# Performance work log

Measured on AMD Instinct MI355X. Metric: run time of the kernel, lower is better.

The kernel has to match this reference:

```python
import jax, jax.numpy as jnp
import numpy as np

M_TOKENS, D_IN, D_OUT = 4096, 4096, 16384


def setup_inputs() -> dict:
    key = jax.random.key(0)
    k1, k2, k3, k4 = jax.random.split(key, 4)
    x = jax.random.normal(k1, (M_TOKENS, D_IN), dtype=jnp.float32)
    # pre-quantized int8 weight, stored [K, N] as in qweight_kn
    qweight_kn = jax.random.randint(k2, (D_IN, D_OUT), -127, 128, dtype=jnp.int8)
    # per-output-channel weight dequant scales (float16 buffer, used as fp32 in kernel)
    weight_scales = jax.random.uniform(k3, (D_OUT,), dtype=jnp.float32, minval=1e-3, maxval=2e-2)
    bias = jax.random.normal(k4, (D_OUT,), dtype=jnp.float32) * 0.01
    return {"x": x, "qweight_kn": qweight_kn, "weight_scales": weight_scales, "bias": bias}


def reference(x, qweight_kn, weight_scales, bias):
    target_dtype = x.dtype
    x2 = x.reshape(-1, x.shape[-1])  # [M, K]
    # dynamic per-token (per-row) symmetric quantization
    x_max = jnp.max(jnp.abs(x2), axis=-1, keepdims=True).astype(jnp.float32) + 1e-5
    x_scales = x_max / 127.0  # [M, 1]
    x_int8 = jnp.clip(jnp.round(x2.astype(jnp.float32) / x_scales), -128, 127).astype(jnp.int8)
    acc = jax.lax.dot_general(
        x_int8, qweight_kn,
        dimension_numbers=(((1,), (0,)), ((), ())),
        preferred_element_type=jnp.int32,
    )  # [M, N] int32
    # fused dequant: row act-scale * col weight-scale, plus bias
    c = acc.astype(jnp.float32) * x_scales * weight_scales[None, :].astype(jnp.float32)
    c = c + bias[None, :]
    out = c.astype(jnp.bfloat16)  # kernel stores bf16
    return out.reshape(*x.shape[:-1], -1).astype(target_dtype)
```

## Files before the change

### kernel.cpp

```cpp
#include <hip/hip_runtime.h>
#include <hip/hip_bf16.h>
#include <stdint.h>

typedef int v4i __attribute__((ext_vector_type(4)));

#define GM 4096
#define GN 16384
#define GK 4096
#define BM 256
#define BN 256
#define BK 64
#define NT (GK / BK)

__device__ __forceinline__ void gload16(const void* g, void* l) {
  __builtin_amdgcn_global_load_lds(
      (const __attribute__((address_space(1))) void*)g,
      (__attribute__((address_space(3))) void*)l, 16, 0, 0);
}

__global__ __launch_bounds__(256) void quant_rows(
    const float* __restrict__ x, int8_t* __restrict__ xq,
    float* __restrict__ xs, int K) {
  const int row = blockIdx.x;
  const int t = threadIdx.x;
  const float4* src = (const float4*)(x + (size_t)row * K) + t * 4;
  float4 v[4];
  float m = 0.f;
#pragma unroll
  for (int i = 0; i < 4; ++i) {
    v[i] = src[i];
    m = fmaxf(m, fmaxf(fmaxf(fabsf(v[i].x), fabsf(v[i].y)),
                       fmaxf(fabsf(v[i].z), fabsf(v[i].w))));
  }
#pragma unroll
  for (int off = 1; off < 64; off <<= 1)
    m = fmaxf(m, __shfl_xor(m, off, 64));
  __shared__ float wmax[4];
  if ((t & 63) == 0) wmax[t >> 6] = m;
  __syncthreads();
  const float gm = fmaxf(fmaxf(wmax[0], wmax[1]), fmaxf(wmax[2], wmax[3]));
  const float scale = (gm + 1e-5f) / 127.0f;
  if (t == 0) xs[row] = scale;
  unsigned packed[4];
#pragma unroll
  for (int i = 0; i < 4; ++i) {
    float fv[4] = {v[i].x, v[i].y, v[i].z, v[i].w};
    unsigned p = 0;
#pragma unroll
    for (int j = 0; j < 4; ++j) {
      int q = (int)rintf(fv[j] / scale);
      q = max(-128, min(127, q));
      p |= (unsigned)(q & 0xff) << (8 * j);
    }
    packed[i] = p;
  }
  *(int4*)(xq + (size_t)row * K + t * 16) =
      make_int4((int)packed[0], (int)packed[1], (int)packed[2], (int)packed[3]);
}

__global__ __launch_bounds__(256) void transpose_pack(
    const int* __restrict__ W32, int8_t* __restrict__ Wt2, int K, int N) {
  __shared__ __align__(16) int8_t tile[64][80];
  const int t = threadIdx.x;
  const int n0 = blockIdx.x * 64;
  const int k0 = blockIdx.y * 64;
  const int ln = t & 63;
  const int wv = t >> 6;
#pragma unroll
  for (int it = 0; it < 16; ++it) {
    const int kk = wv * 16 + it;
    tile[ln][kk] = (int8_t)W32[(size_t)(k0 + kk) * N + n0 + ln];
  }
  __syncthreads();
  const int lane = ln;
  const int4 v = *(const int4*)&tile[wv * 16 + (lane & 15)][(lane >> 4) * 16];
  const int tn = n0 >> 8;
  const int kt = k0 >> 6;
  const int f = ((n0 >> 4) & 15) + wv;
  *(int4*)(Wt2 + (((size_t)(tn * 64 + kt) * 16 + f) * 64 + lane) * 16) = v;
}

__global__ __launch_bounds__(512, 2) void gemm_i8(
    const int8_t* __restrict__ Xq, const int8_t* __restrict__ Wt2,
    const float* __restrict__ xs, const float* __restrict__ wsc,
    const float* __restrict__ bias, float* __restrict__ C) {
  __shared__ __align__(16) int8_t lA[4][BM * BK];

  const int t = threadIdx.x;
  const int lane = t & 63;
  const int w = t >> 6;
  const int wr = w >> 2;
  const int wc = w & 3;
  const int fr = lane & 15;
  const int kg = lane >> 4;

  const int bid = blockIdx.x;
  const int xcd = bid & 7;
  const int q = bid >> 3;
  const int tm = q & 15;
  const int tn = xcd * 8 + (q >> 4);
  const size_t rowA0 = (size_t)tm * BM;
  const size_t rowB0 = (size_t)tn * BN;

  const int8_t* XqB = Xq + rowA0 * GK;
  int srcOff[2], dstOff[2];
#pragma unroll
  for (int i = 0; i < 2; ++i) {
    const int slot0 = (w * 2 + i) * 64;
    const int slot = slot0 + lane;
    const int r = slot >> 2;
    const int c = (slot & 3) ^ ((r >> 2) & 3);
    srcOff[i] = r * GK + c * 16;
    dstOff[i] = slot0 * 16;
  }

#define STAGE(KT, SLOT)                                              \
  {                                                                  \
    const int ko = (KT)*BK;                                          \
    _Pragma("unroll") for (int i = 0; i < 2; ++i)                    \
        gload16(XqB + srcOff[i] + ko, &lA[(SLOT)][0] + dstOff[i]);   \
  }

  const int8_t* bq = Wt2 + (size_t)tn * 1048576 + wc * 4096 + lane * 16;

  v4i acc[8][4] = {};
  v4i areg[8], breg[4][4];

#define LOADB(KT, S)                                                          \
  {                                                                           \
    const int8_t* bp = bq + (size_t)(KT)*16384;                               \
    _Pragma("unroll") for (int nj = 0; nj < 4; ++nj)                          \
        asm volatile("global_load_dwordx4 %0, %1, off"                        \
                     : "=v"(breg[S][nj])                                      \
                     : "v"(bp + nj * 1024)                                    \
                     : "memory");                                             \
  }

  const int ckk = (kg ^ (fr >> 2)) * 16;
#define RD_A(MI, SLOT)                                                        \
  areg[MI] = *(const v4i*)&lA[(SLOT)][(wr * 128 + (MI)*16 + fr) * BK + ckk];

#define SB __builtin_amdgcn_sched_barrier(0)

#define BODY(T, SLOT)                                                         \
  {                                                                           \
         \
    asm volatile("s_waitcnt vmcnt(12)" ::: "memory");                         \
    __builtin_amdgcn_s_barrier();       \
    SB;                                                                       \
    STAGE(((T) + 3) & (NT - 1), ((SLOT) + 3) & 3);                            \
    LOADB(((T) + 3) & (NT - 1), ((SLOT) + 3) & 3);                            \
    SB;                                                                       \
    RD_A(0, SLOT); RD_A(1, SLOT); RD_A(2, SLOT); RD_A(3, SLOT);               \
    SB;                                                                       \
    RD_A(4, SLOT); RD_A(5, SLOT); RD_A(6, SLOT); RD_A(7, SLOT);               \
    SB;                                                                       \
    asm volatile("s_waitcnt lgkmcnt(4)" ::: "memory");        \
    SB;                                                                       \
    __builtin_amdgcn_s_setprio(1);                                            \
    _Pragma("unroll") for (int mi = 0; mi < 4; ++mi)                          \
        _Pragma("unroll") for (int nj = 0; nj < 4; ++nj)                      \
            acc[mi][nj] = __builtin_amdgcn_mfma_i32_16x16x64_i8(              \
                areg[mi], breg[SLOT][nj], acc[mi][nj], 0, 0, 0);              \
    __builtin_amdgcn_s_setprio(0);                                            \
    asm volatile("s_waitcnt lgkmcnt(0)" ::: "memory");        \
    SB;                                                                       \
    __builtin_amdgcn_s_setprio(1);                                            \
    _Pragma("unroll") for (int mi = 4; mi < 8; ++mi)                          \
        _Pragma("unroll") for (int nj = 0; nj < 4; ++nj)                      \
            acc[mi][nj] = __builtin_amdgcn_mfma_i32_16x16x64_i8(              \
                areg[mi], breg[SLOT][nj], acc[mi][nj], 0, 0, 0);              \
    __builtin_amdgcn_s_setprio(0);                                            \
  }

  STAGE(0, 0);
  LOADB(0, 0);
  STAGE(1, 1);
  LOADB(1, 1);
  STAGE(2, 2);
  LOADB(2, 2);

  for (int kt = 0; kt < NT; kt += 4) {
    BODY(kt, 0);
    BODY(kt + 1, 1);
    BODY(kt + 2, 2);
    BODY(kt + 3, 3);
  }
  asm volatile("s_waitcnt vmcnt(0) lgkmcnt(0)" ::: "memory");
  SB;

#pragma unroll
  for (int nj = 0; nj < 4; ++nj) {
    const int col_l = wc * 64 + nj * 16 + fr;
    const float wsv = wsc[rowB0 + col_l];
    const float bv = bias[rowB0 + col_l];
#pragma unroll
    for (int mi = 0; mi < 8; ++mi) {
#pragma unroll
      for (int r = 0; r < 4; ++r) {
        const size_t row = rowA0 + wr * 128 + mi * 16 + kg * 4 + r;
        const float f = (float)acc[mi][nj][r] * xs[row] * wsv + bv;
        C[row * GN + rowB0 + col_l] = __bfloat162float(__float2bfloat16(f));
      }
    }
  }
}

extern "C" void kernel_launch(void* const* d_in, const int* in_sizes, int n_in,
                              void* d_out, int out_size, void* d_ws, size_t ws_size,
                              hipStream_t stream) {
  const int M = GM, K = GK, N = GN;
  const float* x = (const float*)d_in[0];
  const int* W32 = (const int*)d_in[1];
  const float* wsc = (const float*)d_in[2];
  const float* bias = (const float*)d_in[3];
  float* out = (float*)d_out;

  float* xs = (float*)d_ws;
  int8_t* Xq = (int8_t*)d_ws + 16384;
  int8_t* Wt2 = (int8_t*)d_ws + 16384 + (size_t)M * K;

  transpose_pack<<<dim3(N / 64, K / 64), 256, 0, stream>>>(W32, Wt2, K, N);
  quant_rows<<<M, 256, 0, stream>>>(x, Xq, xs, K);
  gemm_i8<<<dim3((M / BM) * (N / BN)), 512, 0, stream>>>(Xq, Wt2, xs, wsc, bias,
                                                         out);
}
```

Baseline: 433.2 us.

## Pre-pack activations into MFMA fragment layout and load A directly to registers

The quantization kernel now writes int8 activations in a tiled fragment-ordered layout matching the MFMA operand order. The GEMM drops the LDS staging of A and loads both A and B straight from global memory into registers with a two-slot pipeline, with no workgroup barriers. This removes LDS traffic and synchronisation, but it loses cross-wave sharing of A tiles, so global/L2 traffic rises. It also doubles register use, and launch bounds drop to one block per CU.

```diff
diff --git a/kernel.cpp b/kernel.cpp
--- a/kernel.cpp
+++ b/kernel.cpp
@@ -12,14 +12,8 @@
 #define BK 64
 #define NT (GK / BK)
 
-__device__ __forceinline__ void gload16(const void* g, void* l) {
-  __builtin_amdgcn_global_load_lds(
-      (const __attribute__((address_space(1))) void*)g,
-      (__attribute__((address_space(3))) void*)l, 16, 0, 0);
-}
-
 __global__ __launch_bounds__(256) void quant_rows(
-    const float* __restrict__ x, int8_t* __restrict__ xq,
+    const float* __restrict__ x, int8_t* __restrict__ xq2,
     float* __restrict__ xs, int K) {
   const int row = blockIdx.x;
   const int t = threadIdx.x;
@@ -54,7 +48,11 @@
     }
     packed[i] = p;
   }
-  *(int4*)(xq + (size_t)row * K + t * 16) =
+  const int tm = row >> 8, f = (row >> 4) & 15, fr = row & 15;
+  const int kt = t >> 2, kg = t & 3;
+  int8_t* dst =
+      xq2 + ((((size_t)(tm * 64 + kt) * 16 + f) * 64) + fr + 16 * kg) * 16;
+  *(int4*)dst =
       make_int4((int)packed[0], (int)packed[1], (int)packed[2], (int)packed[3]);
 }
 
@@ -80,12 +78,10 @@
   *(int4*)(Wt2 + (((size_t)(tn * 64 + kt) * 16 + f) * 64 + lane) * 16) = v;
 }
 
-__global__ __launch_bounds__(512, 2) void gemm_i8(
-    const int8_t* __restrict__ Xq, const int8_t* __restrict__ Wt2,
+__global__ __launch_bounds__(512, 1) void gemm_i8(
+    const int8_t* __restrict__ Xq2, const int8_t* __restrict__ Wt2,
     const float* __restrict__ xs, const float* __restrict__ wsc,
     const float* __restrict__ bias, float* __restrict__ C) {
-  __shared__ __align__(16) int8_t lA[4][BM * BK];
-
   const int t = threadIdx.x;
   const int lane = t & 63;
   const int w = t >> 6;
@@ -102,91 +98,83 @@
   const size_t rowA0 = (size_t)tm * BM;
   const size_t rowB0 = (size_t)tn * BN;
 
-  const int8_t* XqB = Xq + rowA0 * GK;
-  int srcOff[2], dstOff[2];
-#pragma unroll
-  for (int i = 0; i < 2; ++i) {
-    const int slot0 = (w * 2 + i) * 64;
-    const int slot = slot0 + lane;
-    const int r = slot >> 2;
-    const int c = (slot & 3) ^ ((r >> 2) & 3);
-    srcOff[i] = r * GK + c * 16;
-    dstOff[i] = slot0 * 16;
-  }
-
-#define STAGE(KT, SLOT)                                              \
-  {                                                                  \
-    const int ko = (KT)*BK;                                          \
-    _Pragma("unroll") for (int i = 0; i < 2; ++i)                    \
-        gload16(XqB + srcOff[i] + ko, &lA[(SLOT)][0] + dstOff[i]);   \
-  }
-
-  const int8_t* bq = Wt2 + (size_t)tn * 1048576 + wc * 4096 + lane * 16;
+  const int8_t* aq = Xq2 + (size_t)tm * 1048576 + wr * 8192 + (size_t)lane * 16;
+  const int8_t* bq = Wt2 + (size_t)tn * 1048576 + wc * 4096 + (size_t)lane * 16;
 
   v4i acc[8][4] = {};
-  v4i areg[8], breg[4][4];
-
-#define LOADB(KT, S)                                                          \
+  v4i a[2][8], b[2][4];
+
+#define LD(dst, ptr)                                        \
+  asm volatile("global_load_dwordx4 %0, %1, off"            \
+               : "=v"(dst)                                  \
+               : "v"(ptr)                                   \
+               : "memory")
+
+#define LOAD_A_LO(T, S)                                     \
+  {                                                         \
+    const int8_t* p = aq + (size_t)(T)*16384;               \
+    LD(a[S][0], p);                                         \
+    LD(a[S][1], p + 1024);                                  \
+    LD(a[S][2], p + 2048);                                  \
+    LD(a[S][3], p + 3072);                                  \
+  }
+#define LOAD_A_HI(T, S)                                     \
+  {                                                         \
+    const int8_t* p = aq + (size_t)(T)*16384;               \
+    LD(a[S][4], p + 4096);                                  \
+    LD(a[S][5], p + 5120);                                  \
+    LD(a[S][6], p + 6144);                                  \
+    LD(a[S][7], p + 7168);                                  \
+  }
+#define LOAD_B(T, S)                                        \
+  {                                                         \
+    const int8_t* p = bq + (size_t)(T)*16384;               \
+    LD(b[S][0], p);                                         \
+    LD(b[S][1], p + 1024);                                  \
+    LD(b[S][2], p + 2048);                                  \
+    LD(b[S][3], p + 3072);                                  \
+  }
+
+#define SB __builtin_amdgcn_sched_barrier(0)
+
+#define BODY(T, S)                                                            \
   {                                                                           \
-    const int8_t* bp = bq + (size_t)(KT)*16384;                               \
-    _Pragma("unroll") for (int nj = 0; nj < 4; ++nj)                          \
-        asm volatile("global_load_dwordx4 %0, %1, off"                        \
-                     : "=v"(breg[S][nj])                                      \
-                     : "v"(bp + nj * 1024)                                    \
-                     : "memory");                                             \
-  }
-
-  const int ckk = (kg ^ (fr >> 2)) * 16;
-#define RD_A(MI, SLOT)                                                        \
-  areg[MI] = *(const v4i*)&lA[(SLOT)][(wr * 128 + (MI)*16 + fr) * BK + ckk];
-
-#define SB __builtin_amdgcn_sched_barrier(0)
-
-#define BODY(T, SLOT)                                                         \
-  {                                                                           \
-         \
+             \
     asm volatile("s_waitcnt vmcnt(12)" ::: "memory");                         \
-    __builtin_amdgcn_s_barrier();       \
-    SB;                                                                       \
-    STAGE(((T) + 3) & (NT - 1), ((SLOT) + 3) & 3);                            \
-    LOADB(((T) + 3) & (NT - 1), ((SLOT) + 3) & 3);                            \
-    SB;                                                                       \
-    RD_A(0, SLOT); RD_A(1, SLOT); RD_A(2, SLOT); RD_A(3, SLOT);               \
-    SB;                                                                       \
-    RD_A(4, SLOT); RD_A(5, SLOT); RD_A(6, SLOT); RD_A(7, SLOT);               \
-    SB;                                                                       \
-    asm volatile("s_waitcnt lgkmcnt(4)" ::: "memory");        \
     SB;                                                                       \
     __builtin_amdgcn_s_setprio(1);                                            \
     _Pragma("unroll") for (int mi = 0; mi < 4; ++mi)                          \
         _Pragma("unroll") for (int nj = 0; nj < 4; ++nj)                      \
             acc[mi][nj] = __builtin_amdgcn_mfma_i32_16x16x64_i8(              \
-                areg[mi], breg[SLOT][nj], acc[mi][nj], 0, 0, 0);              \
+                a[S][mi], b[S][nj], acc[mi][nj], 0, 0, 0);                    \
     __builtin_amdgcn_s_setprio(0);                                            \
-    asm volatile("s_waitcnt lgkmcnt(0)" ::: "memory");        \
+    SB;                                                                       \
+    LOAD_A_LO(((T) + 2) & (NT - 1), S);              \
     SB;                                                                       \
     __builtin_amdgcn_s_setprio(1);                                            \
     _Pragma("unroll") for (int mi = 4; mi < 8; ++mi)                          \
         _Pragma("unroll") for (int nj = 0; nj < 4; ++nj)                      \
             acc[mi][nj] = __builtin_amdgcn_mfma_i32_16x16x64_i8(              \
-                areg[mi], breg[SLOT][nj], acc[mi][nj], 0, 0, 0);              \
+                a[S][mi], b[S][nj], acc[mi][nj], 0, 0, 0);                    \
     __builtin_amdgcn_s_setprio(0);                                            \
-  }
-
-  STAGE(0, 0);
-  LOADB(0, 0);
-  STAGE(1, 1);
-  LOADB(1, 1);
-  STAGE(2, 2);
-  LOADB(2, 2);
-
-  for (int kt = 0; kt < NT; kt += 4) {
+    SB;                                                                       \
+    LOAD_A_HI(((T) + 2) & (NT - 1), S);        \
+    LOAD_B(((T) + 2) & (NT - 1), S);                                          \
+    SB;                                                                       \
+  }
+
+  LOAD_A_LO(0, 0);
+  LOAD_A_HI(0, 0);
+  LOAD_B(0, 0);
+  LOAD_A_LO(1, 1);
+  LOAD_A_HI(1, 1);
+  LOAD_B(1, 1);
+
+  for (int kt = 0; kt < NT; kt += 2) {
     BODY(kt, 0);
     BODY(kt + 1, 1);
-    BODY(kt + 2, 2);
-    BODY(kt + 3, 3);
-  }
-  asm volatile("s_waitcnt vmcnt(0) lgkmcnt(0)" ::: "memory");
+  }
+  asm volatile("s_waitcnt vmcnt(0)" ::: "memory");
   SB;
 
 #pragma unroll
@@ -217,11 +205,11 @@
   float* out = (float*)d_out;
 
   float* xs = (float*)d_ws;
-  int8_t* Xq = (int8_t*)d_ws + 16384;
+  int8_t* Xq2 = (int8_t*)d_ws + 16384;
   int8_t* Wt2 = (int8_t*)d_ws + 16384 + (size_t)M * K;
 
   transpose_pack<<<dim3(N / 64, K / 64), 256, 0, stream>>>(W32, Wt2, K, N);
-  quant_rows<<<M, 256, 0, stream>>>(x, Xq, xs, K);
-  gemm_i8<<<dim3((M / BM) * (N / BN)), 512, 0, stream>>>(Xq, Wt2, xs, wsc, bias,
+  quant_rows<<<M, 256, 0, stream>>>(x, Xq2, xs, K);
+  gemm_i8<<<dim3((M / BM) * (N / BN)), 512, 0, stream>>>(Xq2, Wt2, xs, wsc, bias,
                                                          out);
 }
```

Result: slower. 470.7 us (+8.7%).

## Pre-pack quantized activations into MFMA fragment layout for contiguous LDS staging

Applied to the files above, without the earlier changes.

The quantization kernel now writes int8 activations directly in a tiled fragment order matching the MFMA operand layout. The GEMM stages A tiles with fully contiguous global-to-LDS copies and reads LDS fragments linearly per lane, with no XOR swizzle. This removes strided row gathers and address arithmetic, and keeps LDS reads free of bank conflicts by construction. In exchange, the quant kernel's global stores become scattered.

```diff
diff --git a/kernel.cpp b/kernel.cpp
--- a/kernel.cpp
+++ b/kernel.cpp
@@ -19,7 +19,7 @@
 }
 
 __global__ __launch_bounds__(256) void quant_rows(
-    const float* __restrict__ x, int8_t* __restrict__ xq,
+    const float* __restrict__ x, int8_t* __restrict__ xq2,
     float* __restrict__ xs, int K) {
   const int row = blockIdx.x;
   const int t = threadIdx.x;
@@ -54,7 +54,11 @@
     }
     packed[i] = p;
   }
-  *(int4*)(xq + (size_t)row * K + t * 16) =
+  const int tm = row >> 8, f = (row >> 4) & 15, fr = row & 15;
+  const int kt = t >> 2, kg = t & 3;
+  int8_t* dst =
+      xq2 + ((((size_t)(tm * 64 + kt) * 16 + f) * 64) + fr + 16 * kg) * 16;
+  *(int4*)dst =
       make_int4((int)packed[0], (int)packed[1], (int)packed[2], (int)packed[3]);
 }
 
@@ -81,10 +85,10 @@
 }
 
 __global__ __launch_bounds__(512, 2) void gemm_i8(
-    const int8_t* __restrict__ Xq, const int8_t* __restrict__ Wt2,
+    const int8_t* __restrict__ Xq2, const int8_t* __restrict__ Wt2,
     const float* __restrict__ xs, const float* __restrict__ wsc,
     const float* __restrict__ bias, float* __restrict__ C) {
-  __shared__ __align__(16) int8_t lA[4][BM * BK];
+  __shared__ __align__(16) int8_t lA[4][16384];
 
   const int t = threadIdx.x;
   const int lane = t & 63;
@@ -102,51 +106,46 @@
   const size_t rowA0 = (size_t)tm * BM;
   const size_t rowB0 = (size_t)tn * BN;
 
-  const int8_t* XqB = Xq + rowA0 * GK;
-  int srcOff[2], dstOff[2];
-#pragma unroll
-  for (int i = 0; i < 2; ++i) {
-    const int slot0 = (w * 2 + i) * 64;
-    const int slot = slot0 + lane;
-    const int r = slot >> 2;
-    const int c = (slot & 3) ^ ((r >> 2) & 3);
-    srcOff[i] = r * GK + c * 16;
-    dstOff[i] = slot0 * 16;
-  }
-
-#define STAGE(KT, SLOT)                                              \
-  {                                                                  \
-    const int ko = (KT)*BK;                                          \
-    _Pragma("unroll") for (int i = 0; i < 2; ++i)                    \
-        gload16(XqB + srcOff[i] + ko, &lA[(SLOT)][0] + dstOff[i]);   \
-  }
-
-  const int8_t* bq = Wt2 + (size_t)tn * 1048576 + wc * 4096 + lane * 16;
+  const int8_t* aqB = Xq2 + (size_t)tm * 1048576 + w * 2048 + (size_t)lane * 16;
+  const int dstO = w * 2048;
+
+#define STAGE(KT, SLOT)                                           \
+  {                                                               \
+    const int8_t* p = aqB + (size_t)(KT)*16384;                   \
+    gload16(p, &lA[(SLOT)][0] + dstO);                            \
+    gload16(p + 1024, &lA[(SLOT)][0] + dstO + 1024);              \
+  }
+
+  const int8_t* bq = Wt2 + (size_t)tn * 1048576 + wc * 4096 + (size_t)lane * 16;
 
   v4i acc[8][4] = {};
   v4i areg[8], breg[4][4];
 
-#define LOADB(KT, S)                                                          \
-  {                                                                           \
-    const int8_t* bp = bq + (size_t)(KT)*16384;                               \
-    _Pragma("unroll") for (int nj = 0; nj < 4; ++nj)                          \
-        asm volatile("global_load_dwordx4 %0, %1, off"                        \
-                     : "=v"(breg[S][nj])                                      \
-                     : "v"(bp + nj * 1024)                                    \
-                     : "memory");                                             \
-  }
-
-  const int ckk = (kg ^ (fr >> 2)) * 16;
-#define RD_A(MI, SLOT)                                                        \
-  areg[MI] = *(const v4i*)&lA[(SLOT)][(wr * 128 + (MI)*16 + fr) * BK + ckk];
+#define LD(dst, ptr)                                        \
+  asm volatile("global_load_dwordx4 %0, %1, off"            \
+               : "=v"(dst)                                  \
+               : "v"(ptr)                                   \
+               : "memory")
+
+#define LOADB(KT, S)                                        \
+  {                                                         \
+    const int8_t* bp = bq + (size_t)(KT)*16384;             \
+    LD(breg[S][0], bp);                                     \
+    LD(breg[S][1], bp + 1024);                              \
+    LD(breg[S][2], bp + 2048);                              \
+    LD(breg[S][3], bp + 3072);                              \
+  }
+
+#define RD_A(MI, SLOT)                                                     \
+  areg[MI] = *(const v4i*)&lA[(SLOT)][(wr * 8 + (MI)) * 1024 + lane * 16];
 
 #define SB __builtin_amdgcn_sched_barrier(0)
 
 #define BODY(T, SLOT)                                                         \
   {                                                                           \
-         \
+                  \
     asm volatile("s_waitcnt vmcnt(12)" ::: "memory");                         \
-    __builtin_amdgcn_s_barrier();       \
+    __builtin_amdgcn_s_barrier();  \
     SB;                                                                       \
     STAGE(((T) + 3) & (NT - 1), ((SLOT) + 3) & 3);                            \
     LOADB(((T) + 3) & (NT - 1), ((SLOT) + 3) & 3);                            \
@@ -217,11 +216,11 @@
   float* out = (float*)d_out;
 
   float* xs = (float*)d_ws;
-  int8_t* Xq = (int8_t*)d_ws + 16384;
+  int8_t* Xq2 = (int8_t*)d_ws + 16384;
   int8_t* Wt2 = (int8_t*)d_ws + 16384 + (size_t)M * K;
 
   transpose_pack<<<dim3(N / 64, K / 64), 256, 0, stream>>>(W32, Wt2, K, N);
-  quant_rows<<<M, 256, 0, stream>>>(x, Xq, xs, K);
-  gemm_i8<<<dim3((M / BM) * (N / BN)), 512, 0, stream>>>(Xq, Wt2, xs, wsc, bias,
+  quant_rows<<<M, 256, 0, stream>>>(x, Xq2, xs, K);
+  gemm_i8<<<dim3((M / BM) * (N / BN)), 512, 0, stream>>>(Xq2, Wt2, xs, wsc, bias,
                                                          out);
 }
```

Measured after the change: 431.8 us. Within noise of the previous version (-0.3%).
